# Performance work log

Hardware: AMD Instinct MI355X
Metric: run time of the kernel (lower is better)

## Reference

```python
import jax, jax.numpy as jnp
import numpy as np

SHRINKAGE = 0.1  # matches init_kwargs shrinkage_rate


def setup_inputs() -> dict:
    key = jax.random.key(0)
    k0, k1, k2, k3 = jax.random.split(key, 4)
    B, F, T, D, P = 8192, 256, 32, 6, 8
    N = 2 ** D - 1  # internal nodes per tree
    L = 2 ** D      # leaves per tree
    return {
        "x": jax.random.normal(k0, (B, F), dtype=jnp.float32),
        "W": jax.random.normal(k1, (T, N, F), dtype=jnp.float32) / np.float32(np.sqrt(F)),
        "b": jax.random.normal(k2, (T, N), dtype=jnp.float32) * 0.01,
        "phi": jax.random.normal(k3, (T, L, P), dtype=jnp.float32),
    }


def reference(x, W, b, phi):
    # x: [B,F]; W: [T,N,F]; b: [T,N]; phi: [T,L,P]
    T, N, F = W.shape
    L = N + 1
    D = int(round(np.log2(L)))
    # all node gating probabilities in one batched GEMM: p(right) per internal node
    s = jax.nn.sigmoid(jnp.einsum('bf,tnf->btn', x, W) + b)  # [B,T,N]
    # heap (level-order) node indexing: node at level d with prefix q has index 2^d-1+q;
    # leaf l's bit at level d is (l >> (D-1-d)) & 1 (1 -> right child -> prob s, 0 -> 1-s)
    leaves = np.arange(L)
    leaf_prob = jnp.ones(s.shape[:2] + (L,), dtype=s.dtype)  # [B,T,L]
    for d in range(D):  # static small loop over tree depth
        bits = jnp.asarray((leaves >> (D - 1 - d)) & 1, dtype=bool)
        idx = (2 ** d - 1) + (leaves >> (D - d))
        sd = s[:, :, idx]  # [B,T,L]
        leaf_prob = leaf_prob * jnp.where(bits, sd, 1.0 - sd)
    # per-tree prediction = sum_l path_prob_l * phi_l; GBM output = shrinkage * sum_t
    tree_pred = jnp.einsum('btl,tlp->btp', leaf_prob, phi)  # [B,T,P]
    return SHRINKAGE * tree_pred.sum(axis=1)  # [B,P]
```

## Files before the change

### kernel.cpp

```cpp
#include <hip/hip_runtime.h>

#define B_TOT   8192
#define F_DIM   256
#define T_TREES 32
#define N_NODES 63
#define P_DIM   8
#define BM      128
#define SHRINK  0.1f

typedef __bf16 bf16_t;
typedef bf16_t bf16x8 __attribute__((ext_vector_type(8)));
typedef float  f32x4  __attribute__((ext_vector_type(4)));
typedef unsigned short ushort8_t __attribute__((ext_vector_type(8)));
typedef unsigned short ushort4_t __attribute__((ext_vector_type(4)));

__device__ __forceinline__ unsigned short f2bf(float f) {
    unsigned int u = __float_as_uint(f);
    u += 0x7fffu + ((u >> 16) & 1u);
    return (unsigned short)(u >> 16);
}
__device__ __forceinline__ float bf2f(unsigned short h) {
    return __uint_as_float(((unsigned int)h) << 16);
}
__device__ __forceinline__ void gl_lds16(const void* g, void* l) {
    __builtin_amdgcn_global_load_lds(
        (const __attribute__((address_space(1))) unsigned int*)g,
        (__attribute__((address_space(3))) unsigned int*)l, 16, 0, 0);
}

__global__ __launch_bounds__(256) void cvt_x(const float* __restrict__ x,
                                             unsigned short* __restrict__ xb) {
    const int i = blockIdx.x * 256 + threadIdx.x;
    const float4 v = *(const float4*)&x[(size_t)i * 4];
    ushort4_t h;
    h.x = f2bf(v.x); h.y = f2bf(v.y); h.z = f2bf(v.z); h.w = f2bf(v.w);
    *(ushort4_t*)&xb[(size_t)i * 4] = h;
}

__global__ __launch_bounds__(256) void cvt_w(const float* __restrict__ W,
                                             unsigned short* __restrict__ Wb) {
    const int i = blockIdx.x * 256 + threadIdx.x;
    const int tree = i >> 12;
    const int rem  = i & 4095;
    const int row  = rem >> 6;
    const int c4   = rem & 63;
    float4 v = make_float4(0.f, 0.f, 0.f, 0.f);
    if (row < N_NODES)
        v = *(const float4*)&W[((size_t)(tree * N_NODES + row)) * F_DIM + c4 * 4];
    ushort4_t h;
    h.x = f2bf(v.x); h.y = f2bf(v.y); h.z = f2bf(v.z); h.w = f2bf(v.w);
    *(ushort4_t*)&Wb[(size_t)i * 4] = h;
}

__global__ __launch_bounds__(256) void cvt_phi(const float* __restrict__ phi,
                                               unsigned short* __restrict__ phiB) {
    const int i = blockIdx.x * 256 + threadIdx.x;
    const int tree = i >> 7;
    const int rem  = i & 127;
    const int k2   = rem >> 6;
    const int lane = rem & 63;
    const int lm   = lane & 15;
    const int quad = lane >> 4;
    ushort8_t h;
#pragma unroll
    for (int j = 0; j < 8; ++j) {
        float v = 0.f;
        if (lm < 8) v = phi[(size_t)tree * 512 + (k2 * 32 + quad * 8 + j) * 8 + lm];
        h[j] = f2bf(v);
    }
    *(ushort8_t*)&phiB[(size_t)i * 8] = h;
}

__global__ __launch_bounds__(256, 2) void softgbm_main(
    const unsigned short* __restrict__ xb, const unsigned short* __restrict__ Wb,
    const unsigned short* __restrict__ phiB, const float* __restrict__ bias,
    float* __restrict__ out)
{
    __shared__ union Smem {
        struct { unsigned short A[BM * 128]; unsigned short B[128 * 128]; } g;
        struct { unsigned short ss[2 * BM * 64]; unsigned short lv[2][BM * 64]; } e;
    } sm;
    __shared__ float bs2[2][64];

    const int tid  = threadIdx.x;
    const int tp   = blockIdx.x;
    const int b0   = blockIdx.y * BM;
    const int wave = tid >> 6;
    const int lane = tid & 63;
    const int quad = lane >> 4;
    const int lm   = lane & 15;
    const int wr   = wave >> 1;
    const int wc   = wave & 1;

    if (tid < 128) {
        const int p = tid >> 6, node = tid & 63;
        bs2[p][node] = (node < N_NODES) ? bias[(tp * 2 + p) * N_NODES + node] : 0.f;
    }

    bf16x8 pb[2][2];
#pragma unroll
    for (int p = 0; p < 2; ++p)
#pragma unroll
        for (int k2 = 0; k2 < 2; ++k2)
            pb[p][k2] = __builtin_bit_cast(bf16x8,
                *(const ushort8_t*)&phiB[(size_t)(((tp * 2 + p) * 2 + k2) * 64 + lane) * 8]);

    f32x4 acc[4][4];
#pragma unroll
    for (int m = 0; m < 4; ++m)
#pragma unroll
        for (int n = 0; n < 4; ++n)
            acc[m][n] = f32x4{0.f, 0.f, 0.f, 0.f};

    for (int ko = 0; ko < F_DIM; ko += 128) {
        __syncthreads();
#pragma unroll
        for (int i = 0; i < 8; ++i) {
            const int r4 = wave * 8 + i;
            const int r  = r4 * 4 + (lane >> 4);
            const int c  = (lane & 15) ^ (r & 7);
            gl_lds16(&xb[(size_t)(b0 + r) * F_DIM + ko + c * 8],
                     (char*)sm.g.A + r4 * 1024);
        }
#pragma unroll
        for (int i = 0; i < 8; ++i) {
            const int r4 = wave * 8 + i;
            const int nr = r4 * 4 + (lane >> 4);
            const int c  = (lane & 15) ^ (nr & 7);
            gl_lds16(&Wb[(size_t)(tp * 128 + nr) * F_DIM + ko + c * 8],
                     (char*)sm.g.B + r4 * 1024);
        }
        __syncthreads();

#pragma unroll
        for (int ks = 0; ks < 4; ++ks) {
            bf16x8 af[4], bf[4];
#pragma unroll
            for (int m = 0; m < 4; ++m) {
                const int r  = wr * 64 + m * 16 + lm;
                const int cp = (ks * 4 + quad) ^ (r & 7);
                af[m] = __builtin_bit_cast(bf16x8, *(ushort8_t*)&sm.g.A[r * 128 + cp * 8]);
            }
#pragma unroll
            for (int n = 0; n < 4; ++n) {
                const int r  = wc * 64 + n * 16 + lm;
                const int cp = (ks * 4 + quad) ^ (r & 7);
                bf[n] = __builtin_bit_cast(bf16x8, *(ushort8_t*)&sm.g.B[r * 128 + cp * 8]);
            }
#pragma unroll
            for (int m = 0; m < 4; ++m)
#pragma unroll
                for (int n = 0; n < 4; ++n)
                    acc[m][n] = __builtin_amdgcn_mfma_f32_16x16x32_bf16(af[m], bf[n], acc[m][n], 0, 0, 0);
        }
    }
    __syncthreads();

#pragma unroll
    for (int m = 0; m < 4; ++m)
#pragma unroll
        for (int n = 0; n < 4; ++n) {
            const int node = n * 16 + lm;
            const float bb = bs2[wc][node];
#pragma unroll
            for (int reg = 0; reg < 4; ++reg) {
                const int row = wr * 64 + m * 16 + quad * 4 + reg;
                const float z = acc[m][n][reg] + bb;
                const float s = 1.0f / (1.0f + __expf(-z));
                const int cp = (node >> 3) ^ (row & 7);
                sm.e.ss[wc * (BM * 64) + row * 64 + cp * 8 + (node & 7)] = f2bf(s);
            }
        }
    __syncthreads();

    f32x4 accp[2] = { f32x4{0.f,0.f,0.f,0.f}, f32x4{0.f,0.f,0.f,0.f} };

    for (int p = 0; p < 2; ++p) {
        {
            const int row = tid >> 1;
            const int h   = tid & 1;
            const unsigned short* sr = &sm.e.ss[p * (BM * 64) + row * 64];
            const int rs = row & 7;
#define RDS(j) bf2f(sr[(((j) >> 3) ^ rs) * 8 + ((j) & 7)])
            const float s0 = RDS(0);
            const float p1 = h ? s0 : (1.0f - s0);
            float q2[2], q3[4], q4[8], q5[16], q6[32];
            {
                const float s = RDS(1 + h);
                q2[0] = p1 * (1.0f - s); q2[1] = p1 * s;
            }
#pragma unroll
            for (int v = 0; v < 2; ++v) {
                const float s = RDS(3 + 2 * h + v);
                q3[2 * v] = q2[v] * (1.0f - s); q3[2 * v + 1] = q2[v] * s;
            }
#pragma unroll
            for (int v = 0; v < 4; ++v) {
                const float s = RDS(7 + 4 * h + v);
                q4[2 * v] = q3[v] * (1.0f - s); q4[2 * v + 1] = q3[v] * s;
            }
#pragma unroll
            for (int v = 0; v < 8; ++v) {
                const float s = RDS(15 + 8 * h + v);
                q5[2 * v] = q4[v] * (1.0f - s); q5[2 * v + 1] = q4[v] * s;
            }
#pragma unroll
            for (int v = 0; v < 16; ++v) {
                const float s = RDS(31 + 16 * h + v);
                q6[2 * v] = q5[v] * (1.0f - s); q6[2 * v + 1] = q5[v] * s;
            }
#undef RDS
            unsigned short* lr = &sm.e.lv[p][row * 64];
#pragma unroll
            for (int j = 0; j < 32; j += 2) {
                const int l  = h * 32 + j;
                const int cp = ((l >> 3) ^ rs);
                const unsigned int pack =
                    (unsigned int)f2bf(q6[j]) | ((unsigned int)f2bf(q6[j + 1]) << 16);
                *(unsigned int*)&lr[cp * 8 + (l & 7)] = pack;
            }
        }
        __syncthreads();

#pragma unroll
        for (int mg = 0; mg < 2; ++mg) {
#pragma unroll
            for (int k2 = 0; k2 < 2; ++k2) {
                const int row = wave * 32 + mg * 16 + lm;
                const int cp  = (k2 * 4 + quad) ^ (row & 7);
                const bf16x8 afr = __builtin_bit_cast(bf16x8,
                    *(ushort8_t*)&sm.e.lv[p][row * 64 + cp * 8]);
                accp[mg] = __builtin_amdgcn_mfma_f32_16x16x32_bf16(afr, pb[p][k2], accp[mg], 0, 0, 0);
            }
        }
    }

    if (lm < P_DIM) {
#pragma unroll
        for (int mg = 0; mg < 2; ++mg)
#pragma unroll
            for (int reg = 0; reg < 4; ++reg) {
                const int row = wave * 32 + mg * 16 + quad * 4 + reg;
                atomicAdd(&out[(size_t)(b0 + row) * P_DIM + lm], SHRINK * accp[mg][reg]);
            }
    }
}

extern "C" void kernel_launch(void* const* d_in, const int* in_sizes, int n_in,
                              void* d_out, int out_size, void* d_ws, size_t ws_size,
                              hipStream_t stream) {
    const float* x    = (const float*)d_in[0];
    const float* W    = (const float*)d_in[1];
    const float* bias = (const float*)d_in[2];
    const float* phi  = (const float*)d_in[3];
    float* out = (float*)d_out;

    unsigned short* xb   = (unsigned short*)d_ws;
    unsigned short* Wb   = xb + (size_t)B_TOT * F_DIM;
    unsigned short* phiB = Wb + (size_t)T_TREES * 64 * F_DIM;

    cvt_x  <<<dim3((B_TOT * F_DIM / 4) / 256), dim3(256), 0, stream>>>(x, xb);
    cvt_w  <<<dim3((T_TREES * 64 * F_DIM / 4) / 256), dim3(256), 0, stream>>>(W, Wb);
    cvt_phi<<<dim3(16), dim3(256), 0, stream>>>(phi, phiB);
    hipMemsetAsync(out, 0, sizeof(float) * B_TOT * P_DIM, stream);

    dim3 grid(T_TREES / 2, B_TOT / BM);
    softgbm_main<<<grid, dim3(256), 0, stream>>>(xb, Wb, phiB, bias, out);
}
```

Baseline: 96.42 us.

## Merge conversion kernels, shrink GEMM K-tile and LDS, vectorize leaf-probability stage

Folds the three bf16 conversion kernels into one launch. Halves the GEMM K-tile to 64 so shared memory shrinks and occupancy can rise to three blocks per CU, and reuses a single leaf buffer. The sigmoid outputs are now read as wide vector loads and unpacked in registers, the complementary child probability is formed by subtraction instead of a second multiply, and bf16 packing uses 128-bit stores. The costs are more K-loop iterations and barriers, an extra sync per tree, and tighter register pressure under the higher launch-bounds target.

Measured after the change: 91.45 us. 1.05x faster.

```diff
diff --git a/kernel.cpp b/kernel.cpp
--- a/kernel.cpp
+++ b/kernel.cpp
@@ -19,8 +19,10 @@
     u += 0x7fffu + ((u >> 16) & 1u);
     return (unsigned short)(u >> 16);
 }
-__device__ __forceinline__ float bf2f(unsigned short h) {
-    return __uint_as_float(((unsigned int)h) << 16);
+__device__ __forceinline__ unsigned int pk2bf(float a, float b) {
+    unsigned int ua = __float_as_uint(a); ua += 0x7fffu + ((ua >> 16) & 1u);
+    unsigned int ub = __float_as_uint(b); ub += 0x7fffu + ((ub >> 16) & 1u);
+    return (ua >> 16) | (ub & 0xffff0000u);
 }
 __device__ __forceinline__ void gl_lds16(const void* g, void* l) {
     __builtin_amdgcn_global_load_lds(
@@ -28,58 +30,61 @@
         (__attribute__((address_space(3))) unsigned int*)l, 16, 0, 0);
 }
 
-__global__ __launch_bounds__(256) void cvt_x(const float* __restrict__ x,
-                                             unsigned short* __restrict__ xb) {
-    const int i = blockIdx.x * 256 + threadIdx.x;
-    const float4 v = *(const float4*)&x[(size_t)i * 4];
-    ushort4_t h;
-    h.x = f2bf(v.x); h.y = f2bf(v.y); h.z = f2bf(v.z); h.w = f2bf(v.w);
-    *(ushort4_t*)&xb[(size_t)i * 4] = h;
-}
-
-__global__ __launch_bounds__(256) void cvt_w(const float* __restrict__ W,
-                                             unsigned short* __restrict__ Wb) {
-    const int i = blockIdx.x * 256 + threadIdx.x;
-    const int tree = i >> 12;
-    const int rem  = i & 4095;
-    const int row  = rem >> 6;
-    const int c4   = rem & 63;
-    float4 v = make_float4(0.f, 0.f, 0.f, 0.f);
-    if (row < N_NODES)
-        v = *(const float4*)&W[((size_t)(tree * N_NODES + row)) * F_DIM + c4 * 4];
-    ushort4_t h;
-    h.x = f2bf(v.x); h.y = f2bf(v.y); h.z = f2bf(v.z); h.w = f2bf(v.w);
-    *(ushort4_t*)&Wb[(size_t)i * 4] = h;
-}
-
-__global__ __launch_bounds__(256) void cvt_phi(const float* __restrict__ phi,
-                                               unsigned short* __restrict__ phiB) {
-    const int i = blockIdx.x * 256 + threadIdx.x;
-    const int tree = i >> 7;
-    const int rem  = i & 127;
-    const int k2   = rem >> 6;
-    const int lane = rem & 63;
-    const int lm   = lane & 15;
-    const int quad = lane >> 4;
-    ushort8_t h;
-#pragma unroll
-    for (int j = 0; j < 8; ++j) {
-        float v = 0.f;
-        if (lm < 8) v = phi[(size_t)tree * 512 + (k2 * 32 + quad * 8 + j) * 8 + lm];
-        h[j] = f2bf(v);
-    }
-    *(ushort8_t*)&phiB[(size_t)i * 8] = h;
-}
-
-__global__ __launch_bounds__(256, 2) void softgbm_main(
+__global__ __launch_bounds__(256) void cvt_all(
+    const float* __restrict__ x, const float* __restrict__ W,
+    const float* __restrict__ phi,
+    unsigned short* __restrict__ xb, unsigned short* __restrict__ Wb,
+    unsigned short* __restrict__ phiB)
+{
+    const int bx  = blockIdx.x;
+    const int tid = threadIdx.x;
+    if (bx < 2048) {
+        const int i = bx * 256 + tid;
+        const float4 v = *(const float4*)&x[(size_t)i * 4];
+        ushort4_t h;
+        h.x = f2bf(v.x); h.y = f2bf(v.y); h.z = f2bf(v.z); h.w = f2bf(v.w);
+        *(ushort4_t*)&xb[(size_t)i * 4] = h;
+    } else if (bx < 2560) {
+        const int i = (bx - 2048) * 256 + tid;
+        const int tree = i >> 12;
+        const int rem  = i & 4095;
+        const int row  = rem >> 6;
+        const int c4   = rem & 63;
+        float4 v = make_float4(0.f, 0.f, 0.f, 0.f);
+        if (row < N_NODES)
+            v = *(const float4*)&W[((size_t)(tree * N_NODES + row)) * F_DIM + c4 * 4];
+        ushort4_t h;
+        h.x = f2bf(v.x); h.y = f2bf(v.y); h.z = f2bf(v.z); h.w = f2bf(v.w);
+        *(ushort4_t*)&Wb[(size_t)i * 4] = h;
+    } else {
+        const int i = (bx - 2560) * 256 + tid;
+        const int tree = i >> 7;
+        const int rem  = i & 127;
+        const int k2   = rem >> 6;
+        const int lane = rem & 63;
+        const int lm   = lane & 15;
+        const int quad = lane >> 4;
+        ushort8_t h;
+#pragma unroll
+        for (int j = 0; j < 8; ++j) {
+            float v = 0.f;
+            if (lm < 8) v = phi[(size_t)tree * 512 + (k2 * 32 + quad * 8 + j) * 8 + lm];
+            h[j] = f2bf(v);
+        }
+        *(ushort8_t*)&phiB[(size_t)i * 8] = h;
+    }
+}
+
+__global__ __launch_bounds__(256, 3) void softgbm_main(
     const unsigned short* __restrict__ xb, const unsigned short* __restrict__ Wb,
     const unsigned short* __restrict__ phiB, const float* __restrict__ bias,
     float* __restrict__ out)
 {
     __shared__ union Smem {
-        struct { unsigned short A[BM * 128]; unsigned short B[128 * 128]; } g;
-        struct { unsigned short ss[2 * BM * 64]; unsigned short lv[2][BM * 64]; } e;
+        struct { unsigned short A[BM * 64]; unsigned short B[BM * 64]; } g;
+        unsigned short ss[2][BM * 64];
     } sm;
+    __shared__ unsigned short lv[BM * 64];
     __shared__ float bs2[2][64];
 
     const int tid  = threadIdx.x;
@@ -97,6 +102,55 @@
         bs2[p][node] = (node < N_NODES) ? bias[(tp * 2 + p) * N_NODES + node] : 0.f;
     }
 
+    f32x4 acc[4][4];
+#pragma unroll
+    for (int m = 0; m < 4; ++m)
+#pragma unroll
+        for (int n = 0; n < 4; ++n)
+            acc[m][n] = f32x4{0.f, 0.f, 0.f, 0.f};
+
+    for (int ko = 0; ko < F_DIM; ko += 64) {
+        __syncthreads();
+#pragma unroll
+        for (int i = 0; i < 4; ++i) {
+            const int r = wave * 32 + i * 8 + (lane >> 3);
+            const int c = (lane & 7) ^ (r & 7);
+            gl_lds16(&xb[(size_t)(b0 + r) * F_DIM + ko + c * 8],
+                     &sm.g.A[(wave * 32 + i * 8) * 64]);
+        }
+#pragma unroll
+        for (int i = 0; i < 4; ++i) {
+            const int r = wave * 32 + i * 8 + (lane >> 3);
+            const int c = (lane & 7) ^ (r & 7);
+            gl_lds16(&Wb[(size_t)(tp * 128 + r) * F_DIM + ko + c * 8],
+                     &sm.g.B[(wave * 32 + i * 8) * 64]);
+        }
+        __syncthreads();
+
+#pragma unroll
+        for (int ks = 0; ks < 2; ++ks) {
+            bf16x8 af[4], bfr[4];
+#pragma unroll
+            for (int m = 0; m < 4; ++m) {
+                const int r  = wr * 64 + m * 16 + lm;
+                const int cp = (ks * 4 + quad) ^ (r & 7);
+                af[m] = __builtin_bit_cast(bf16x8, *(ushort8_t*)&sm.g.A[r * 64 + cp * 8]);
+            }
+#pragma unroll
+            for (int n = 0; n < 4; ++n) {
+                const int r  = wc * 64 + n * 16 + lm;
+                const int cp = (ks * 4 + quad) ^ (r & 7);
+                bfr[n] = __builtin_bit_cast(bf16x8, *(ushort8_t*)&sm.g.B[r * 64 + cp * 8]);
+            }
+#pragma unroll
+            for (int m = 0; m < 4; ++m)
+#pragma unroll
+                for (int n = 0; n < 4; ++n)
+                    acc[m][n] = __builtin_amdgcn_mfma_f32_16x16x32_bf16(af[m], bfr[n], acc[m][n], 0, 0, 0);
+        }
+    }
+    __syncthreads();
+
     bf16x8 pb[2][2];
 #pragma unroll
     for (int p = 0; p < 2; ++p)
@@ -105,57 +159,6 @@
             pb[p][k2] = __builtin_bit_cast(bf16x8,
                 *(const ushort8_t*)&phiB[(size_t)(((tp * 2 + p) * 2 + k2) * 64 + lane) * 8]);
 
-    f32x4 acc[4][4];
-#pragma unroll
-    for (int m = 0; m < 4; ++m)
-#pragma unroll
-        for (int n = 0; n < 4; ++n)
-            acc[m][n] = f32x4{0.f, 0.f, 0.f, 0.f};
-
-    for (int ko = 0; ko < F_DIM; ko += 128) {
-        __syncthreads();
-#pragma unroll
-        for (int i = 0; i < 8; ++i) {
-            const int r4 = wave * 8 + i;
-            const int r  = r4 * 4 + (lane >> 4);
-            const int c  = (lane & 15) ^ (r & 7);
-            gl_lds16(&xb[(size_t)(b0 + r) * F_DIM + ko + c * 8],
-                     (char*)sm.g.A + r4 * 1024);
-        }
-#pragma unroll
-        for (int i = 0; i < 8; ++i) {
-            const int r4 = wave * 8 + i;
-            const int nr = r4 * 4 + (lane >> 4);
-            const int c  = (lane & 15) ^ (nr & 7);
-            gl_lds16(&Wb[(size_t)(tp * 128 + nr) * F_DIM + ko + c * 8],
-                     (char*)sm.g.B + r4 * 1024);
-        }
-        __syncthreads();
-
-#pragma unroll
-        for (int ks = 0; ks < 4; ++ks) {
-            bf16x8 af[4], bf[4];
-#pragma unroll
-            for (int m = 0; m < 4; ++m) {
-                const int r  = wr * 64 + m * 16 + lm;
-                const int cp = (ks * 4 + quad) ^ (r & 7);
-                af[m] = __builtin_bit_cast(bf16x8, *(ushort8_t*)&sm.g.A[r * 128 + cp * 8]);
-            }
-#pragma unroll
-            for (int n = 0; n < 4; ++n) {
-                const int r  = wc * 64 + n * 16 + lm;
-                const int cp = (ks * 4 + quad) ^ (r & 7);
-                bf[n] = __builtin_bit_cast(bf16x8, *(ushort8_t*)&sm.g.B[r * 128 + cp * 8]);
-            }
-#pragma unroll
-            for (int m = 0; m < 4; ++m)
-#pragma unroll
-                for (int n = 0; n < 4; ++n)
-                    acc[m][n] = __builtin_amdgcn_mfma_f32_16x16x32_bf16(af[m], bf[n], acc[m][n], 0, 0, 0);
-        }
-    }
-    __syncthreads();
-
 #pragma unroll
     for (int m = 0; m < 4; ++m)
 #pragma unroll
@@ -166,59 +169,66 @@
             for (int reg = 0; reg < 4; ++reg) {
                 const int row = wr * 64 + m * 16 + quad * 4 + reg;
                 const float z = acc[m][n][reg] + bb;
-                const float s = 1.0f / (1.0f + __expf(-z));
-                const int cp = (node >> 3) ^ (row & 7);
-                sm.e.ss[wc * (BM * 64) + row * 64 + cp * 8 + (node & 7)] = f2bf(s);
+                const float s = __frcp_rn(1.0f + __expf(-z));
+                const int slot = (node >> 3) ^ (row & 7);
+                sm.ss[wc][row * 64 + slot * 8 + (node & 7)] = f2bf(s);
             }
         }
     __syncthreads();
 
     f32x4 accp[2] = { f32x4{0.f,0.f,0.f,0.f}, f32x4{0.f,0.f,0.f,0.f} };
 
+    const int row = tid >> 1;
+    const int h   = tid & 1;
+    const int rs  = row & 7;
+
     for (int p = 0; p < 2; ++p) {
+        const unsigned short* sp = &sm.ss[p][row * 64];
+        unsigned int cw[32];
+#pragma unroll
+        for (int c = 0; c < 8; ++c)
+            *(uint4*)&cw[c * 4] = *(const uint4*)&sp[(c ^ rs) * 8];
+
+#define NV(j) ((j) & 1 ? __uint_as_float(cw[(j) >> 1] & 0xffff0000u) \
+                       : __uint_as_float(cw[(j) >> 1] << 16))
+#define SEL(a, b) (h ? NV(b) : NV(a))
+        const float s0v = NV(0);
+        const float q1  = h ? s0v : (1.0f - s0v);
+        float q2[2], q3[4], q4[8], q5[16], q6[32];
         {
-            const int row = tid >> 1;
-            const int h   = tid & 1;
-            const unsigned short* sr = &sm.e.ss[p * (BM * 64) + row * 64];
-            const int rs = row & 7;
-#define RDS(j) bf2f(sr[(((j) >> 3) ^ rs) * 8 + ((j) & 7)])
-            const float s0 = RDS(0);
-            const float p1 = h ? s0 : (1.0f - s0);
-            float q2[2], q3[4], q4[8], q5[16], q6[32];
-            {
-                const float s = RDS(1 + h);
-                q2[0] = p1 * (1.0f - s); q2[1] = p1 * s;
-            }
-#pragma unroll
-            for (int v = 0; v < 2; ++v) {
-                const float s = RDS(3 + 2 * h + v);
-                q3[2 * v] = q2[v] * (1.0f - s); q3[2 * v + 1] = q2[v] * s;
-            }
-#pragma unroll
-            for (int v = 0; v < 4; ++v) {
-                const float s = RDS(7 + 4 * h + v);
-                q4[2 * v] = q3[v] * (1.0f - s); q4[2 * v + 1] = q3[v] * s;
-            }
-#pragma unroll
-            for (int v = 0; v < 8; ++v) {
-                const float s = RDS(15 + 8 * h + v);
-                q5[2 * v] = q4[v] * (1.0f - s); q5[2 * v + 1] = q4[v] * s;
-            }
-#pragma unroll
-            for (int v = 0; v < 16; ++v) {
-                const float s = RDS(31 + 16 * h + v);
-                q6[2 * v] = q5[v] * (1.0f - s); q6[2 * v + 1] = q5[v] * s;
-            }
-#undef RDS
-            unsigned short* lr = &sm.e.lv[p][row * 64];
-#pragma unroll
-            for (int j = 0; j < 32; j += 2) {
-                const int l  = h * 32 + j;
-                const int cp = ((l >> 3) ^ rs);
-                const unsigned int pack =
-                    (unsigned int)f2bf(q6[j]) | ((unsigned int)f2bf(q6[j + 1]) << 16);
-                *(unsigned int*)&lr[cp * 8 + (l & 7)] = pack;
-            }
+            const float t = SEL(1, 2);
+            q2[1] = q1 * t; q2[0] = q1 - q2[1];
+        }
+#pragma unroll
+        for (int v = 0; v < 2; ++v) {
+            const float t = SEL(3 + v, 5 + v);
+            q3[2 * v + 1] = q2[v] * t; q3[2 * v] = q2[v] - q3[2 * v + 1];
+        }
+#pragma unroll
+        for (int v = 0; v < 4; ++v) {
+            const float t = SEL(7 + v, 11 + v);
+            q4[2 * v + 1] = q3[v] * t; q4[2 * v] = q3[v] - q4[2 * v + 1];
+        }
+#pragma unroll
+        for (int v = 0; v < 8; ++v) {
+            const float t = SEL(15 + v, 23 + v);
+            q5[2 * v + 1] = q4[v] * t; q5[2 * v] = q4[v] - q5[2 * v + 1];
+        }
+#pragma unroll
+        for (int v = 0; v < 16; ++v) {
+            const float t = SEL(31 + v, 47 + v);
+            q6[2 * v + 1] = q5[v] * t; q6[2 * v] = q5[v] - q6[2 * v + 1];
+        }
+#undef SEL
+#undef NV
+#pragma unroll
+        for (int i = 0; i < 4; ++i) {
+            uint4 w;
+            w.x = pk2bf(q6[i * 8 + 0], q6[i * 8 + 1]);
+            w.y = pk2bf(q6[i * 8 + 2], q6[i * 8 + 3]);
+            w.z = pk2bf(q6[i * 8 + 4], q6[i * 8 + 5]);
+            w.w = pk2bf(q6[i * 8 + 6], q6[i * 8 + 7]);
+            *(uint4*)&lv[row * 64 + (((h * 4 + i) ^ rs)) * 8] = w;
         }
         __syncthreads();
 
@@ -226,13 +236,14 @@
         for (int mg = 0; mg < 2; ++mg) {
 #pragma unroll
             for (int k2 = 0; k2 < 2; ++k2) {
-                const int row = wave * 32 + mg * 16 + lm;
-                const int cp  = (k2 * 4 + quad) ^ (row & 7);
+                const int r2 = wave * 32 + mg * 16 + lm;
+                const int cp = (k2 * 4 + quad) ^ (r2 & 7);
                 const bf16x8 afr = __builtin_bit_cast(bf16x8,
-                    *(ushort8_t*)&sm.e.lv[p][row * 64 + cp * 8]);
+                    *(ushort8_t*)&lv[r2 * 64 + cp * 8]);
                 accp[mg] = __builtin_amdgcn_mfma_f32_16x16x32_bf16(afr, pb[p][k2], accp[mg], 0, 0, 0);
             }
         }
+        __syncthreads();
     }
 
     if (lm < P_DIM) {
@@ -240,8 +251,8 @@
         for (int mg = 0; mg < 2; ++mg)
 #pragma unroll
             for (int reg = 0; reg < 4; ++reg) {
-                const int row = wave * 32 + mg * 16 + quad * 4 + reg;
-                atomicAdd(&out[(size_t)(b0 + row) * P_DIM + lm], SHRINK * accp[mg][reg]);
+                const int r2 = wave * 32 + mg * 16 + quad * 4 + reg;
+                atomicAdd(&out[(size_t)(b0 + r2) * P_DIM + lm], SHRINK * accp[mg][reg]);
             }
     }
 }
@@ -259,10 +270,8 @@
     unsigned short* Wb   = xb + (size_t)B_TOT * F_DIM;
     unsigned short* phiB = Wb + (size_t)T_TREES * 64 * F_DIM;
 
-    cvt_x  <<<dim3((B_TOT * F_DIM / 4) / 256), dim3(256), 0, stream>>>(x, xb);
-    cvt_w  <<<dim3((T_TREES * 64 * F_DIM / 4) / 256), dim3(256), 0, stream>>>(W, Wb);
-    cvt_phi<<<dim3(16), dim3(256), 0, stream>>>(phi, phiB);
     hipMemsetAsync(out, 0, sizeof(float) * B_TOT * P_DIM, stream);
+    cvt_all<<<dim3(2576), dim3(256), 0, stream>>>(x, W, phi, xb, Wb, phiB);
 
     dim3 grid(T_TREES / 2, B_TOT / BM);
     softgbm_main<<<grid, dim3(256), 0, stream>>>(xb, Wb, phiB, bias, out);
```
